# Performance work log

Hardware: AMD Instinct MI355X
Metric: run time of the kernel (lower is better)

The kernel has to match this reference:

```python
import jax, jax.numpy as jnp
import numpy as np

HEAD_SCALE = 1
REAR_SCALE = 3
MAX_CLIP_NUM = 64


def _prop3d(x):
    # x: [B, ns, D, nc]
    B, ns, D, nc = x.shape
    scale_range = REAR_SCALE - HEAD_SCALE + 2
    bases = [2 ** i for i in range(HEAD_SCALE - 1, REAR_SCALE + 2)]
    map_hidden = jnp.zeros((B, D, scale_range, nc, nc + 1), x.dtype)
    map_mask = jnp.zeros((B, D, scale_range, nc, nc + 1), x.dtype)
    for rel_idx in range(scale_range):
        base = bases[rel_idx]
        step = MAX_CLIP_NUM // base
        abs_idx = rel_idx + HEAD_SCALE - 1
        now = x[:, abs_idx]  # [B, D, nc]
        for step_idx in range(1, step + 1):
            if step_idx > 1:
                # MaxPool1d(kernel=2, stride=1): length shrinks by 1
                now = jnp.maximum(now[..., :-1], now[..., 1:])
            # proposals of length step_idx*base starting at multiples of base
            starts = np.arange(0, nc - step_idx * base, base)
            if starts.size == 0:
                break
            ends = starts + step_idx * base  # column index in [0, nc]
            vals = now[..., starts]  # [B, D, n_props] gather at proposal starts
            map_hidden = map_hidden.at[:, :, rel_idx, starts, ends].set(vals)
            map_mask = map_mask.at[:, :, rel_idx, starts, ends].set(jnp.asarray(1.0, x.dtype))
    return map_hidden, map_mask


def setup_inputs() -> dict:
    key = jax.random.key(0)
    x = jax.random.normal(key, (8, 4, 512, 64), dtype=jnp.float32)
    return {"x": x}


def reference(x):
    return _prop3d(x)
```

## Files before the change

### kernel.cpp

```cpp
#include <hip/hip_runtime.h>


#define HIDDEN_ELEMS 68157440LL

typedef float vfloat4 __attribute__((ext_vector_type(4)));

__global__ __launch_bounds__(256) void prop3d_kernel(const float* __restrict__ x,
                                                     float* __restrict__ out) {
    const int gid = blockIdx.x;
    const int rel = gid & 3;
    const int d   = (gid >> 2) & 511;
    const int bi  = gid >> 11;
    const int t   = threadIdx.x;

    __shared__ float ST[64][6];

    const float* xr = x + (((long long)(bi * 4 + rel)) * 512 + d) * 64;

    if (t < 64) {
        float v = xr[t];
        ST[t][0] = v;
        #pragma unroll
        for (int p = 1; p < 6; ++p) {
            int j = t + (1 << (p - 1));
            j = j > 63 ? 63 : j;
            float o = __shfl(v, j, 64);
            v = fmaxf(v, o);
            ST[t][p] = v;
        }
    }
    __syncthreads();

    const int bmask = (1 << rel) - 1;

    vfloat4* __restrict__ outH = reinterpret_cast<vfloat4*>(out) + (long long)gid * 1040;
    vfloat4* __restrict__ outM = reinterpret_cast<vfloat4*>(out + HIDDEN_ELEMS) + (long long)gid * 1040;

    for (int idx = t; idx < 1040; idx += 256) {
        const int f0 = idx * 4;
        vfloat4 v, mv;
        #pragma unroll
        for (int u = 0; u < 4; ++u) {
            const int f = f0 + u;
            const int s = f / 65;
            const int e = f - s * 65;
            const int diff = e - s;
            const bool valid = (e < 64) & (diff > 0) &
                               ((s & bmask) == 0) & ((diff & bmask) == 0);
            const int k  = diff >> rel;
            const int kk = valid ? k : 1;
            const int p  = 31 - __clz(kk);
            const float a = ST[s][p];
            const float c = ST[s + kk - (1 << p)][p];
            const float m = fmaxf(a, c);
            v[u]  = valid ? m : 0.0f;
            mv[u] = valid ? 1.0f : 0.0f;
        }
        outH[idx] = v;
        outM[idx] = mv;
    }
}

extern "C" void kernel_launch(void* const* d_in, const int* in_sizes, int n_in,
                              void* d_out, int out_size, void* d_ws, size_t ws_size,
                              hipStream_t stream) {
    const float* x = (const float*)d_in[0];
    float* out = (float*)d_out;
    prop3d_kernel<<<16384, 256, 0, stream>>>(x, out);
}
```

Baseline: 534.8 us.

## Process eight rows per block and hoist index math into registers

```diff
diff --git a/kernel.cpp b/kernel.cpp
--- a/kernel.cpp
+++ b/kernel.cpp
@@ -7,57 +7,98 @@
 
 __global__ __launch_bounds__(256) void prop3d_kernel(const float* __restrict__ x,
                                                      float* __restrict__ out) {
-    const int gid = blockIdx.x;
-    const int rel = gid & 3;
-    const int d   = (gid >> 2) & 511;
-    const int bi  = gid >> 11;
     const int t   = threadIdx.x;
+    const int b   = blockIdx.x;
+    const int rel = b & 3;
+    const int j0  = (b >> 2) * 8;
+    const int bmask = (1 << rel) - 1;
+
+    int aw[5][4];
+    unsigned vmask = 0;
+    #pragma unroll
+    for (int j = 0; j < 5; ++j) {
+        #pragma unroll
+        for (int u = 0; u < 4; ++u) {
+            const int f = (t + j * 256) * 4 + u;
+            int w = 0;
+            if (f < 4160) {
+                const int s = f / 65;
+                const int e = f - s * 65;
+                const int diff = e - s;
+                const bool valid = (e < 64) & (diff > 0) &
+                                   ((s & bmask) == 0) & ((diff & bmask) == 0);
+                const int k  = diff >> rel;
+                const int kk = valid ? k : 1;
+                const int p  = 31 - __clz(kk);
+                const int a1 = s * 6 + p;
+                const int a2 = (s + kk - (1 << p)) * 6 + p;
+                w = a1 | (a2 << 16);
+                vmask |= (valid ? 1u : 0u) << (j * 4 + u);
+            }
+            aw[j][u] = w;
+        }
+    }
 
     __shared__ float ST[64][6];
+    const float* __restrict__ stb = &ST[0][0];
 
-    const float* xr = x + (((long long)(bi * 4 + rel)) * 512 + d) * 64;
+    const int bi = j0 >> 9;
+    const int d0 = j0 & 511;
+    const float* __restrict__ xbase = x + (((long long)(bi * 4 + rel)) * 512 + d0) * 64;
 
-    if (t < 64) {
-        float v = xr[t];
-        ST[t][0] = v;
+    for (int r = 0; r < 8; ++r) {
+        __syncthreads();
+        if (t < 64) {
+            float v = xbase[r * 64 + t];
+            ST[t][0] = v;
+            #pragma unroll
+            for (int p = 1; p < 6; ++p) {
+                int jj = t + (1 << (p - 1));
+                jj = jj > 63 ? 63 : jj;
+                float o = __shfl(v, jj, 64);
+                v = fmaxf(v, o);
+                ST[t][p] = v;
+            }
+        }
+        __syncthreads();
+
+        const long long gid = (long long)(j0 + r) * 4 + rel;
+        vfloat4* __restrict__ outH = reinterpret_cast<vfloat4*>(out) + gid * 1040;
         #pragma unroll
-        for (int p = 1; p < 6; ++p) {
-            int j = t + (1 << (p - 1));
-            j = j > 63 ? 63 : j;
-            float o = __shfl(v, j, 64);
-            v = fmaxf(v, o);
-            ST[t][p] = v;
+        for (int j = 0; j < 5; ++j) {
+            const int idx = t + j * 256;
+            if (idx < 1040) {
+                vfloat4 v;
+                #pragma unroll
+                for (int u = 0; u < 4; ++u) {
+                    const int w = aw[j][u];
+                    const float a = stb[w & 0xffff];
+                    const float c = stb[w >> 16];
+                    const float m = fmaxf(a, c);
+                    v[u] = ((vmask >> (j * 4 + u)) & 1) ? m : 0.0f;
+                }
+                outH[idx] = v;
+            }
         }
     }
-    __syncthreads();
 
-    const int bmask = (1 << rel) - 1;
-
-    vfloat4* __restrict__ outH = reinterpret_cast<vfloat4*>(out) + (long long)gid * 1040;
-    vfloat4* __restrict__ outM = reinterpret_cast<vfloat4*>(out + HIDDEN_ELEMS) + (long long)gid * 1040;
-
-    for (int idx = t; idx < 1040; idx += 256) {
-        const int f0 = idx * 4;
-        vfloat4 v, mv;
+    vfloat4 mpat[5];
+    #pragma unroll
+    for (int j = 0; j < 5; ++j) {
         #pragma unroll
-        for (int u = 0; u < 4; ++u) {
-            const int f = f0 + u;
-            const int s = f / 65;
-            const int e = f - s * 65;
-            const int diff = e - s;
-            const bool valid = (e < 64) & (diff > 0) &
-                               ((s & bmask) == 0) & ((diff & bmask) == 0);
-            const int k  = diff >> rel;
-            const int kk = valid ? k : 1;
-            const int p  = 31 - __clz(kk);
-            const float a = ST[s][p];
-            const float c = ST[s + kk - (1 << p)][p];
-            const float m = fmaxf(a, c);
-            v[u]  = valid ? m : 0.0f;
-            mv[u] = valid ? 1.0f : 0.0f;
+        for (int u = 0; u < 4; ++u)
+            mpat[j][u] = ((vmask >> (j * 4 + u)) & 1) ? 1.0f : 0.0f;
+    }
+    #pragma unroll
+    for (int r = 0; r < 8; ++r) {
+        const long long gid = (long long)(j0 + r) * 4 + rel;
+        vfloat4* __restrict__ outM =
+            reinterpret_cast<vfloat4*>(out + HIDDEN_ELEMS) + gid * 1040;
+        #pragma unroll
+        for (int j = 0; j < 5; ++j) {
+            const int idx = t + j * 256;
+            if (idx < 1040) outM[idx] = mpat[j];
         }
-        outH[idx] = v;
-        outM[idx] = mv;
     }
 }
 
@@ -66,5 +107,5 @@
                               hipStream_t stream) {
     const float* x = (const float*)d_in[0];
     float* out = (float*)d_out;
-    prop3d_kernel<<<16384, 256, 0, stream>>>(x, out);
+    prop3d_kernel<<<2048, 256, 0, stream>>>(x, out);
 }
```

New measurement: 537.5 us. About the same (+0.5%).

## Zero output with memset and scatter only upper-triangle proposal entries

Applied to the files above, without the earlier changes.

```diff
diff --git a/kernel.cpp b/kernel.cpp
--- a/kernel.cpp
+++ b/kernel.cpp
@@ -3,61 +3,52 @@
 
 #define HIDDEN_ELEMS 68157440LL
 
-typedef float vfloat4 __attribute__((ext_vector_type(4)));
+__global__ __launch_bounds__(256) void prop3d_scatter(const float* __restrict__ x,
+                                                      float* __restrict__ out) {
+    const int blk  = blockIdx.x;
+    const int bi   = blk >> 9;
+    const int d    = blk & 511;
+    const int t    = threadIdx.x;
+    const int rel  = t >> 6;
+    const int lane = t & 63;
+    const int b    = 1 << rel;
+    const int bmask = b - 1;
 
-__global__ __launch_bounds__(256) void prop3d_kernel(const float* __restrict__ x,
-                                                     float* __restrict__ out) {
-    const int gid = blockIdx.x;
-    const int rel = gid & 3;
-    const int d   = (gid >> 2) & 511;
-    const int bi  = gid >> 11;
-    const int t   = threadIdx.x;
+    __shared__ float ST[4][64][6];
 
-    __shared__ float ST[64][6];
-
-    const float* xr = x + (((long long)(bi * 4 + rel)) * 512 + d) * 64;
-
-    if (t < 64) {
-        float v = xr[t];
-        ST[t][0] = v;
+    const float* __restrict__ xr = x + (((long long)(bi * 4 + rel)) * 512 + d) * 64;
+    {
+        float v = xr[lane];
+        ST[rel][lane][0] = v;
         #pragma unroll
         for (int p = 1; p < 6; ++p) {
-            int j = t + (1 << (p - 1));
-            j = j > 63 ? 63 : j;
-            float o = __shfl(v, j, 64);
+            int jj = lane + (1 << (p - 1));
+            jj = jj > 63 ? 63 : jj;
+            float o = __shfl(v, jj, 64);
             v = fmaxf(v, o);
-            ST[t][p] = v;
+            ST[rel][lane][p] = v;
         }
     }
-    __syncthreads();
 
-    const int bmask = (1 << rel) - 1;
+    const long long gbase = ((long long)blk * 4 + rel) * 4160;
+    float* __restrict__ outH = out + gbase;
+    float* __restrict__ outM = out + HIDDEN_ELEMS + gbase;
 
-    vfloat4* __restrict__ outH = reinterpret_cast<vfloat4*>(out) + (long long)gid * 1040;
-    vfloat4* __restrict__ outM = reinterpret_cast<vfloat4*>(out + HIDDEN_ELEMS) + (long long)gid * 1040;
-
-    for (int idx = t; idx < 1040; idx += 256) {
-        const int f0 = idx * 4;
-        vfloat4 v, mv;
-        #pragma unroll
-        for (int u = 0; u < 4; ++u) {
-            const int f = f0 + u;
-            const int s = f / 65;
-            const int e = f - s * 65;
-            const int diff = e - s;
-            const bool valid = (e < 64) & (diff > 0) &
-                               ((s & bmask) == 0) & ((diff & bmask) == 0);
+    for (int s = 0; s + b < 64; s += b) {
+        const int c = s + b + lane;
+        if (c <= 63) {
+            const int diff = c - s;
+            const bool valid = (diff & bmask) == 0;
             const int k  = diff >> rel;
             const int kk = valid ? k : 1;
             const int p  = 31 - __clz(kk);
-            const float a = ST[s][p];
-            const float c = ST[s + kk - (1 << p)][p];
-            const float m = fmaxf(a, c);
-            v[u]  = valid ? m : 0.0f;
-            mv[u] = valid ? 1.0f : 0.0f;
+            const float a  = ST[rel][s][p];
+            const float c2 = ST[rel][s + kk - (1 << p)][p];
+            const float m  = fmaxf(a, c2);
+            const int o = s * 65 + c;
+            outH[o] = valid ? m : 0.0f;
+            outM[o] = valid ? 1.0f : 0.0f;
         }
-        outH[idx] = v;
-        outM[idx] = mv;
     }
 }
 
@@ -66,5 +57,6 @@
                               hipStream_t stream) {
     const float* x = (const float*)d_in[0];
     float* out = (float*)d_out;
-    prop3d_kernel<<<16384, 256, 0, stream>>>(x, out);
+    hipMemsetAsync(d_out, 0, (size_t)out_size, stream);
+    prop3d_scatter<<<4096, 256, 0, stream>>>(x, out);
 }
```

New measurement: 564.7 us. 5.6% more time.
